# Optimization experiments

Measured on AMD Instinct MI355X. Metric: run time of the kernel, lower is better.

Reference implementation:

```python
import jax, jax.numpy as jnp
import numpy as np
import math

DIM = 1024
HEADS = 16
WINDOW = 256  # window_size; also used as block size (band covers 3 blocks)


def _rope(x):
    # canonical half-split RoPE over the FULL feature dim (as the module applies
    # it before the head split), base 10000
    b, s, d = x.shape
    half = d // 2
    inv_freq = 1.0 / (10000.0 ** (jnp.arange(half, dtype=jnp.float32) / half))
    ang = jnp.arange(s, dtype=jnp.float32)[:, None] * inv_freq[None, :]  # [s, half]
    cos, sin = jnp.cos(ang), jnp.sin(ang)
    x1, x2 = x[..., :half], x[..., half:]
    return jnp.concatenate([x1 * cos - x2 * sin, x1 * sin + x2 * cos], axis=-1)


def setup_inputs() -> dict:
    key = jax.random.key(0)
    ks = jax.random.split(key, 8)
    d = DIM
    q = jax.random.normal(ks[0], (2, 4096, d), dtype=jnp.float32)
    k = jax.random.normal(ks[1], (2, 4096, d), dtype=jnp.float32)
    v = jax.random.normal(ks[2], (2, 4096, d), dtype=jnp.float32)
    wq = jax.random.normal(ks[3], (d, d), dtype=jnp.float32) * 0.02
    wk = jax.random.normal(ks[4], (d, d), dtype=jnp.float32) * 0.02
    wv = jax.random.normal(ks[5], (d, d), dtype=jnp.float32) * 0.02
    wo_w = jax.random.normal(ks[6], (d, d), dtype=jnp.float32) * 0.02
    wo_b = jnp.zeros((d,), dtype=jnp.float32)
    return {"q": q, "k": k, "v": v, "wq": wq, "wk": wk, "wv": wv,
            "wo_w": wo_w, "wo_b": wo_b}


def reference(q, k, v, wq, wk, wv, wo_w, wo_b):
    b, s, d = q.shape
    h, W = HEADS, WINDOW
    dk = d // h
    B = W                      # block size == window -> band of 3 blocks
    nb = s // B

    # projections (torch Linear: x @ W^T), then RoPE over the full dim
    qp = _rope(jnp.einsum('bsd,ed->bse', q, wq))
    kp = _rope(jnp.einsum('bsd,ed->bse', k, wk))
    vp = jnp.einsum('bsd,ed->bse', v, wv)

    # split heads -> [b, h, s, dk]
    qh = qp.reshape(b, s, h, dk).transpose(0, 2, 1, 3)
    kh = kp.reshape(b, s, h, dk).transpose(0, 2, 1, 3)
    vh = vp.reshape(b, s, h, dk).transpose(0, 2, 1, 3)

    # pad keys/values by one block on each side, gather 3-block bands
    kpad = jnp.pad(kh, ((0, 0), (0, 0), (B, B), (0, 0)))
    vpad = jnp.pad(vh, ((0, 0), (0, 0), (B, B), (0, 0)))
    kblk = kpad.reshape(b, h, nb + 2, B, dk)
    vblk = vpad.reshape(b, h, nb + 2, B, dk)
    kband = jnp.concatenate([kblk[:, :, i:i + nb] for i in range(3)], axis=3)  # [b,h,nb,3B,dk]
    vband = jnp.concatenate([vblk[:, :, i:i + nb] for i in range(3)], axis=3)

    qb = qh.reshape(b, h, nb, B, dk)
    # NOTE: original multiplies by sqrt(dim_k) (not divides) -- kept faithfully
    scores = jnp.einsum('bhnqd,bhnkd->bhnqk', qb, kband) * math.sqrt(dk)

    # band mask: key global pos = (n-1)*B + ki, query global pos = n*B + qi
    n_idx = jnp.arange(nb)[:, None, None]
    qi = jnp.arange(B)[None, :, None]
    ki = jnp.arange(3 * B)[None, None, :]
    kpos = (n_idx - 1) * B + ki
    rel = ki - B - qi  # key_pos - query_pos
    valid = (rel >= -W) & (rel <= W) & (kpos >= 0) & (kpos < s)  # [nb,B,3B]

    neg = jnp.asarray(jnp.finfo(scores.dtype).min, scores.dtype)
    scores = jnp.where(valid[None, None], scores, neg)
    attn = jax.nn.softmax(scores, axis=-1)

    out = jnp.einsum('bhnqk,bhnkd->bhnqd', attn, vband)
    out = out.reshape(b, h, s, dk).transpose(0, 2, 1, 3).reshape(b, s, d)
    return jnp.einsum('bsd,ed->bse', out, wo_w) + wo_b
```

## Files before the change

### kernel.cpp

```cpp
#include <hip/hip_runtime.h>


typedef __attribute__((ext_vector_type(8))) short short8v;
typedef __attribute__((ext_vector_type(4))) float float4v;
typedef __attribute__((ext_vector_type(8))) _Float16 half8v;

#define MFMA_BF16(A_, B_, C_) __builtin_amdgcn_mfma_f32_16x16x32_bf16((A_), (B_), (C_), 0, 0, 0)
#define MFMA_F16(A_, B_, C_)  __builtin_amdgcn_mfma_f32_16x16x32_f16((A_), (B_), (C_), 0, 0, 0)

__device__ __forceinline__ void split_rn(float x, short& h, short& l) {
    unsigned int u = __float_as_uint(x);
    u += 0x7fffu + ((u >> 16) & 1u);
    unsigned int hb = u & 0xffff0000u;
    h = (short)(hb >> 16);
    float lo = x - __uint_as_float(hb);
    l = (short)(__float_as_uint(lo) >> 16);
}

__device__ __forceinline__ void dma16(const void* g, void* l) {
    __builtin_amdgcn_global_load_lds(
        (__attribute__((address_space(1))) void*)g,
        (__attribute__((address_space(3))) void*)l, 16, 0, 0);
}

__global__ __launch_bounds__(256) void prep_k(
    const float* __restrict__ wq, const float* __restrict__ wk,
    const float* __restrict__ wv, unsigned short* __restrict__ scr)
{
    const int M1 = 1 << 20;
    unsigned int tid = blockIdx.x * 256 + threadIdx.x;
    if (tid < (unsigned)M1) {
        short h, l; split_rn(wq[tid], h, l);
        scr[tid] = (unsigned short)h;
        scr[M1 + tid] = (unsigned short)l;
    } else if (tid < (unsigned)(2 * M1)) {
        unsigned int i = tid - M1;
        short h, l; split_rn(wk[i], h, l);
        scr[2 * M1 + i] = (unsigned short)h;
        scr[3 * M1 + i] = (unsigned short)l;
    } else {
        unsigned int i = tid - 2 * M1;
        scr[4 * M1 + i] = __builtin_bit_cast(unsigned short, (_Float16)wv[i]);
    }
}

__global__ __launch_bounds__(256) void gemm_qk(
    const float* __restrict__ A0, const short* __restrict__ Bh0,
    const short* __restrict__ Bl0, float* __restrict__ C0,
    const float* __restrict__ A1, const short* __restrict__ Bh1,
    const short* __restrict__ Bl1, float* __restrict__ C1)
{
    const int N = 1024, K = 1024;
    const float* Ap = blockIdx.z ? A1 : A0;
    const short* Bhp = blockIdx.z ? Bh1 : Bh0;
    const short* Blp = blockIdx.z ? Bl1 : Bl0;
    float*       Cp = blockIdx.z ? C1 : C0;

    __shared__ __align__(16) short Ahs[128 * 32];
    __shared__ __align__(16) short Als[128 * 32];
    __shared__ __align__(16) short Bhs[128 * 32];
    __shared__ __align__(16) short Bls[128 * 32];

    const int t = threadIdx.x;
    const int bm = blockIdx.y << 7;
    const int bn = blockIdx.x << 7;
    const int lane = t & 63;
    const int wave = t >> 6;
    const int wm = (wave >> 1) << 6;
    const int wn = (wave & 1) << 6;
    const int c16 = lane & 15;
    const int quad = lane >> 4;
    const int lr = t >> 2;
    const int lc = (t & 3) << 3;

    float4v acc[4][4];
#pragma unroll
    for (int i = 0; i < 4; i++)
#pragma unroll
        for (int j = 0; j < 4; j++) acc[i][j] = (float4v){0.f, 0.f, 0.f, 0.f};

    for (int kb = 0; kb < K; kb += 32) {
#pragma unroll
        for (int g = 0; g < 2; g++) {
            size_t off = (size_t)(bn + g * 64 + lr) * K + kb + lc;
            dma16(Bhp + off, Bhs + g * 2048 + wave * 512);
            dma16(Blp + off, Bls + g * 2048 + wave * 512);
        }
#pragma unroll
        for (int g = 0; g < 2; g++) {
            const float* src = Ap + (size_t)(bm + g * 64 + lr) * K + kb + lc;
            float4v f0 = *(const float4v*)src;
            float4v f1 = *(const float4v*)(src + 4);
            short8v h, l;
#pragma unroll
            for (int j = 0; j < 8; j++) {
                float x = (j < 4) ? f0[j] : f1[j - 4];
                short hh, ll; split_rn(x, hh, ll);
                h[j] = hh; l[j] = ll;
            }
            *(short8v*)(Ahs + (g * 64 + lr) * 32 + lc) = h;
            *(short8v*)(Als + (g * 64 + lr) * 32 + lc) = l;
        }
        __syncthreads();

        short8v ah[4], al[4], bh[4], bl[4];
#pragma unroll
        for (int i = 0; i < 4; i++) {
            ah[i] = *(const short8v*)(Ahs + (wm + i * 16 + c16) * 32 + quad * 8);
            al[i] = *(const short8v*)(Als + (wm + i * 16 + c16) * 32 + quad * 8);
        }
#pragma unroll
        for (int j = 0; j < 4; j++) {
            bh[j] = *(const short8v*)(Bhs + (wn + j * 16 + c16) * 32 + quad * 8);
            bl[j] = *(const short8v*)(Bls + (wn + j * 16 + c16) * 32 + quad * 8);
        }
#pragma unroll
        for (int i = 0; i < 4; i++)
#pragma unroll
            for (int j = 0; j < 4; j++) {
                acc[i][j] = MFMA_BF16(ah[i], bh[j], acc[i][j]);
                acc[i][j] = MFMA_BF16(ah[i], bl[j], acc[i][j]);
                acc[i][j] = MFMA_BF16(al[i], bh[j], acc[i][j]);
            }
        __syncthreads();
    }

#pragma unroll
    for (int i = 0; i < 4; i++)
#pragma unroll
        for (int j = 0; j < 4; j++)
#pragma unroll
            for (int r = 0; r < 4; r++) {
                int gr = bm + wm + i * 16 + quad * 4 + r;
                int gc = bn + wn + j * 16 + c16;
                Cp[(size_t)gr * N + gc] = acc[i][j][r];
            }
}

template <int AF16, int BF16, int OMODE>
__global__ __launch_bounds__(256) void gemm16(
    const void* __restrict__ Ap, const void* __restrict__ Bp,
    void* __restrict__ Cp, const float* __restrict__ bias)
{
    const int N = 1024, K = 1024;

    __shared__ __align__(16) short As[128 * 32];
    __shared__ __align__(16) short Bs[128 * 32];

    const int t = threadIdx.x;
    const int bm = blockIdx.y << 7;
    const int bn = blockIdx.x << 7;
    const int lane = t & 63;
    const int wave = t >> 6;
    const int wm = (wave >> 1) << 6;
    const int wn = (wave & 1) << 6;
    const int c16 = lane & 15;
    const int quad = lane >> 4;
    const int lr = t >> 2;
    const int lc = (t & 3) << 3;

    float4v acc[4][4];
#pragma unroll
    for (int i = 0; i < 4; i++)
#pragma unroll
        for (int j = 0; j < 4; j++) acc[i][j] = (float4v){0.f, 0.f, 0.f, 0.f};

    for (int kb = 0; kb < K; kb += 32) {
        if (AF16) {
            const _Float16* Af = (const _Float16*)Ap;
#pragma unroll
            for (int g = 0; g < 2; g++)
                dma16(Af + (size_t)(bm + g * 64 + lr) * K + kb + lc,
                      As + g * 2048 + wave * 512);
        } else {
            const float* Af = (const float*)Ap;
#pragma unroll
            for (int g = 0; g < 2; g++) {
                const float* src = Af + (size_t)(bm + g * 64 + lr) * K + kb + lc;
                float4v f0 = *(const float4v*)src;
                float4v f1 = *(const float4v*)(src + 4);
                half8v h;
#pragma unroll
                for (int j = 0; j < 8; j++) h[j] = (_Float16)((j < 4) ? f0[j] : f1[j - 4]);
                *(half8v*)(As + (g * 64 + lr) * 32 + lc) = h;
            }
        }
        if (BF16) {
            const _Float16* Bf = (const _Float16*)Bp;
#pragma unroll
            for (int g = 0; g < 2; g++)
                dma16(Bf + (size_t)(bn + g * 64 + lr) * K + kb + lc,
                      Bs + g * 2048 + wave * 512);
        } else {
            const float* Bf = (const float*)Bp;
#pragma unroll
            for (int g = 0; g < 2; g++) {
                const float* src = Bf + (size_t)(bn + g * 64 + lr) * K + kb + lc;
                float4v f0 = *(const float4v*)src;
                float4v f1 = *(const float4v*)(src + 4);
                half8v h;
#pragma unroll
                for (int j = 0; j < 8; j++) h[j] = (_Float16)((j < 4) ? f0[j] : f1[j - 4]);
                *(half8v*)(Bs + (g * 64 + lr) * 32 + lc) = h;
            }
        }
        __syncthreads();

        half8v ah[4], bh[4];
#pragma unroll
        for (int i = 0; i < 4; i++)
            ah[i] = *(const half8v*)(As + (wm + i * 16 + c16) * 32 + quad * 8);
#pragma unroll
        for (int j = 0; j < 4; j++)
            bh[j] = *(const half8v*)(Bs + (wn + j * 16 + c16) * 32 + quad * 8);
#pragma unroll
        for (int i = 0; i < 4; i++)
#pragma unroll
            for (int j = 0; j < 4; j++)
                acc[i][j] = MFMA_F16(ah[i], bh[j], acc[i][j]);
        __syncthreads();
    }

#pragma unroll
    for (int i = 0; i < 4; i++)
#pragma unroll
        for (int j = 0; j < 4; j++)
#pragma unroll
            for (int r = 0; r < 4; r++) {
                int gr = bm + wm + i * 16 + quad * 4 + r;
                int gc = bn + wn + j * 16 + c16;
                float vv = acc[i][j][r];
                if (OMODE == 0) {
                    ((unsigned short*)Cp)[((size_t)(gc << 1) + (gr >> 12)) * 4096 + (gr & 4095)] =
                        __builtin_bit_cast(unsigned short, (_Float16)vv);
                } else {
                    ((float*)Cp)[(size_t)gr * N + gc] = vv + bias[gc];
                }
            }
}

__global__ __launch_bounds__(256) void rope_pack(float* __restrict__ QP, float* __restrict__ KP)
{
    int sp = blockIdx.x;
    int t = threadIdx.x;
    float* rows[4] = { QP + ((size_t)sp << 10), QP + ((size_t)(4096 + sp) << 10),
                       KP + ((size_t)sp << 10), KP + ((size_t)(4096 + sp) << 10) };

    float c[2], sn[2];
    float x1[4][2], x2[4][2];
#pragma unroll
    for (int p = 0; p < 2; p++) {
        int j = t + p * 256;
        float freq = __expf(-0.017988946f * (float)j);
        float ang = (float)sp * freq;
        sincosf(ang, &sn[p], &c[p]);
#pragma unroll
        for (int r = 0; r < 4; r++) {
            x1[r][p] = rows[r][j];
            x2[r][p] = rows[r][j + 512];
        }
    }
    __syncthreads();
#pragma unroll
    for (int r = 0; r < 4; r++) {
        unsigned short* u = (unsigned short*)rows[r];
#pragma unroll
        for (int p = 0; p < 2; p++) {
            int j = t + p * 256;
            float y1 = x1[r][p] * c[p] - x2[r][p] * sn[p];
            float y2 = x1[r][p] * sn[p] + x2[r][p] * c[p];
            short h1, l1, h2, l2;
            split_rn(y1, h1, l1);
            split_rn(y2, h2, l2);
            u[j] = (unsigned short)h1;
            u[j + 512] = (unsigned short)h2;
            u[1024 + j] = (unsigned short)l1;
            u[1024 + j + 512] = (unsigned short)l2;
        }
    }
}

__global__ __launch_bounds__(256) void attn_k(
    const unsigned short* __restrict__ QHL, const unsigned short* __restrict__ KHL,
    const unsigned short* __restrict__ VT, unsigned short* __restrict__ AO)
{
    const int S = 4096;
    const float NEG = -1e30f;
    const float PSC = 512.0f;
    const int bq = blockIdx.x, h = blockIdx.y, b = blockIdx.z;
    const int t = threadIdx.x;
    const int wave = t >> 6, lane = t & 63;
    const int col = lane & 15, quad = lane >> 4;
    const int qg = (bq << 6) + (wave << 4);

    __shared__ __align__(16) short Khs[64 * 72];
    __shared__ __align__(16) short Kls[64 * 72];
    __shared__ __align__(16) short Vs[64 * 72];
    __shared__ __align__(16) short Ps[4][16 * 72];
    short* myP = &Ps[wave][0];

    const int sk = t >> 3;
    const int sd = (t & 7) << 3;

    short8v qh[2], ql[2];
    {
        const unsigned short* qr = QHL + ((size_t)(b * S + qg + col) << 11) + h * 64 + quad * 8;
        qh[0] = *(const short8v*)(qr);
        qh[1] = *(const short8v*)(qr + 32);
        ql[0] = *(const short8v*)(qr + 1024);
        ql[1] = *(const short8v*)(qr + 1024 + 32);
    }

    float mrun[4], lrun[4];
    float4v O[4];
#pragma unroll
    for (int r = 0; r < 4; r++) { mrun[r] = NEG; lrun[r] = 0.f; }
#pragma unroll
    for (int t4 = 0; t4 < 4; t4++) O[t4] = (float4v){0.f, 0.f, 0.f, 0.f};

    const int blk0 = bq << 6;
    const int kstart = (blk0 - 256 > 0) ? (blk0 - 256) : 0;
    const int kend = (blk0 + 320 < S) ? (blk0 + 320) : S;

    for (int kb = kstart; kb < kend; kb += 64) {
#pragma unroll
        for (int p = 0; p < 2; p++) {
            int key = p * 32 + sk;
            const unsigned short* krow = KHL + ((size_t)(b * S + kb + key) << 11) + h * 64 + sd;
            *(short8v*)(Khs + key * 72 + sd) = *(const short8v*)krow;
            *(short8v*)(Kls + key * 72 + sd) = *(const short8v*)(krow + 1024);
            int dm = p * 32 + sk;
            const unsigned short* vrow = VT + ((size_t)((h * 64 + dm) << 1) + b) * S + kb + sd;
            *(short8v*)(Vs + dm * 72 + sd) = *(const short8v*)vrow;
        }
        __syncthreads();

        float4v sv[4];
#pragma unroll
        for (int c = 0; c < 4; c++) {
            const short* kro = Khs + (c * 16 + col) * 72 + quad * 8;
            const short* klo = Kls + (c * 16 + col) * 72 + quad * 8;
            short8v kh0 = *(const short8v*)kro;
            short8v kh1 = *(const short8v*)(kro + 32);
            short8v kl0 = *(const short8v*)klo;
            short8v kl1 = *(const short8v*)(klo + 32);
            float4v sc = (float4v){0.f, 0.f, 0.f, 0.f};
            sc = MFMA_BF16(qh[0], kh0, sc);
            sc = MFMA_BF16(qh[1], kh1, sc);
            sc = MFMA_BF16(qh[0], kl0, sc);
            sc = MFMA_BF16(qh[1], kl1, sc);
            sc = MFMA_BF16(ql[0], kh0, sc);
            sc = MFMA_BF16(ql[1], kh1, sc);
            sv[c] = sc;
        }

        float mx[4], alpha[4], psum[4];
#pragma unroll
        for (int r = 0; r < 4; r++) {
            int qrow = qg + quad * 4 + r;
            float m = NEG;
#pragma unroll
            for (int c = 0; c < 4; c++) {
                int key = kb + c * 16 + col;
                float vv = (key >= qrow - 256 && key <= qrow + 256) ? sv[c][r] * 8.0f : NEG;
                sv[c][r] = vv;
                m = fmaxf(m, vv);
            }
            mx[r] = m;
        }
#pragma unroll
        for (int st = 1; st < 16; st <<= 1)
#pragma unroll
            for (int r = 0; r < 4; r++) mx[r] = fmaxf(mx[r], __shfl_xor(mx[r], st, 64));

#pragma unroll
        for (int r = 0; r < 4; r++) {
            float mn = fmaxf(mrun[r], mx[r]);
            alpha[r] = __expf(mrun[r] - mn);
            mrun[r] = mn;
            float ps = 0.f;
#pragma unroll
            for (int c = 0; c < 4; c++) {
                float p = __expf(sv[c][r] - mn);
                ps += p;
                myP[(quad * 4 + r) * 72 + c * 16 + col] =
                    __builtin_bit_cast(short, (_Float16)(p * PSC));
            }
            psum[r] = ps;
        }
#pragma unroll
        for (int st = 1; st < 16; st <<= 1)
#pragma unroll
            for (int r = 0; r < 4; r++) psum[r] += __shfl_xor(psum[r], st, 64);
#pragma unroll
        for (int r = 0; r < 4; r++) lrun[r] = lrun[r] * alpha[r] + psum[r];
#pragma unroll
        for (int t4 = 0; t4 < 4; t4++)
#pragma unroll
            for (int r = 0; r < 4; r++) O[t4][r] *= alpha[r];

#pragma unroll
        for (int kf = 0; kf < 2; kf++) {
            half8v pa = *(const half8v*)(myP + col * 72 + kf * 32 + quad * 8);
#pragma unroll
            for (int t4 = 0; t4 < 4; t4++) {
                half8v vb = *(const half8v*)(Vs + (t4 * 16 + col) * 72 + kf * 32 + quad * 8);
                O[t4] = MFMA_F16(pa, vb, O[t4]);
            }
        }
        __syncthreads();
    }

#pragma unroll
    for (int r = 0; r < 4; r++) {
        float inv = (lrun[r] > 0.f) ? (1.0f / (lrun[r] * PSC)) : 0.f;
        unsigned short* orow = AO + (size_t)(b * S + qg + quad * 4 + r) * 1024 + h * 64;
#pragma unroll
        for (int t4 = 0; t4 < 4; t4++)
            orow[t4 * 16 + col] = __builtin_bit_cast(unsigned short, (_Float16)(O[t4][r] * inv));
    }
}

extern "C" void kernel_launch(void* const* d_in, const int* in_sizes, int n_in,
                              void* d_out, int out_size, void* d_ws, size_t ws_size,
                              hipStream_t stream) {
    const float* q   = (const float*)d_in[0];
    const float* k   = (const float*)d_in[1];
    const float* v   = (const float*)d_in[2];
    const float* wq  = (const float*)d_in[3];
    const float* wk  = (const float*)d_in[4];
    const float* wv  = (const float*)d_in[5];
    const float* wo  = (const float*)d_in[6];
    const float* wob = (const float*)d_in[7];

    float* QP = (float*)d_ws;
    float* KP = QP + (size_t)8192 * 1024;
    unsigned short* VT = (unsigned short*)(KP + (size_t)8192 * 1024);
    unsigned short* AO = VT + (size_t)8192 * 1024;

    unsigned short* scr = (unsigned short*)d_out;
    const int M1 = 1 << 20;
    const short* wqh = (const short*)(scr);
    const short* wql = (const short*)(scr + M1);
    const short* wkh = (const short*)(scr + 2 * M1);
    const short* wkl = (const short*)(scr + 3 * M1);
    const void*  wv16 = (const void*)(scr + 4 * M1);

    prep_k<<<12288, 256, 0, stream>>>(wq, wk, wv, scr);
    gemm_qk<<<dim3(8, 64, 2), 256, 0, stream>>>(q, wqh, wql, QP, k, wkh, wkl, KP);
    rope_pack<<<4096, 256, 0, stream>>>(QP, KP);
    gemm16<0, 1, 0><<<dim3(8, 64), 256, 0, stream>>>(v, wv16, (void*)VT, nullptr);
    attn_k<<<dim3(64, 16, 2), 256, 0, stream>>>((const unsigned short*)QP,
                                                (const unsigned short*)KP, VT, AO);
    gemm16<1, 0, 1><<<dim3(8, 64), 256, 0, stream>>>(AO, wo, d_out, wob);
}
```

Measured before the change: 457.1 us.

## Rewrite split-bf16 Q/K projection GEMM with 256x256 tiles and double-buffered LDS

Replaces the 128x128 Q/K projection GEMM with a 512-thread, 256x256-tile kernel. It double-buffers LDS, prefetches the next A tile into registers and DMAs the next B tile while computing, and paces the loads with explicit vmcnt waits and barriers. It also adds an XOR swizzle to avoid LDS bank conflicts, an XCD-aware block remap, and raised MFMA priority. The goal is to hide global-load latency and raise MFMA utilisation, at the cost of higher register and LDS pressure and fragile hand-tuned wait counts.

```diff
diff --git a/kernel.cpp b/kernel.cpp
--- a/kernel.cpp
+++ b/kernel.cpp
@@ -7,6 +7,11 @@
 
 #define MFMA_BF16(A_, B_, C_) __builtin_amdgcn_mfma_f32_16x16x32_bf16((A_), (B_), (C_), 0, 0, 0)
 #define MFMA_F16(A_, B_, C_)  __builtin_amdgcn_mfma_f32_16x16x32_f16((A_), (B_), (C_), 0, 0, 0)
+
+#define VMW_(n) asm volatile("s_waitcnt vmcnt(" #n ")" ::: "memory")
+#define VMW(n) VMW_(n)
+#define LGKM0 asm volatile("s_waitcnt lgkmcnt(0)" ::: "memory")
+#define BARF do { __builtin_amdgcn_s_barrier(); asm volatile("" ::: "memory"); } while (0)
 
 __device__ __forceinline__ void split_rn(float x, short& h, short& l) {
     unsigned int u = __float_as_uint(x);
@@ -44,97 +49,187 @@
     }
 }
 
-__global__ __launch_bounds__(256) void gemm_qk(
+__global__ __launch_bounds__(512, 2) void gemm_qk2(
     const float* __restrict__ A0, const short* __restrict__ Bh0,
     const short* __restrict__ Bl0, float* __restrict__ C0,
     const float* __restrict__ A1, const short* __restrict__ Bh1,
     const short* __restrict__ Bl1, float* __restrict__ C1)
 {
-    const int N = 1024, K = 1024;
-    const float* Ap = blockIdx.z ? A1 : A0;
-    const short* Bhp = blockIdx.z ? Bh1 : Bh0;
-    const short* Blp = blockIdx.z ? Bl1 : Bl0;
-    float*       Cp = blockIdx.z ? C1 : C0;
-
-    __shared__ __align__(16) short Ahs[128 * 32];
-    __shared__ __align__(16) short Als[128 * 32];
-    __shared__ __align__(16) short Bhs[128 * 32];
-    __shared__ __align__(16) short Bls[128 * 32];
+    __shared__ __align__(16) short S[2 * 32768];
+
+    const int bid = blockIdx.x;
+    const int cid = ((bid & 7) << 5) | (bid >> 3);
+    const int z   = cid >> 7;
+    const int rem = cid & 127;
+    const int bm  = (rem >> 2) << 8;
+    const int bn  = (rem & 3) << 8;
+
+    const float* Ap  = z ? A1  : A0;
+    const short* Bhp = z ? Bh1 : Bh0;
+    const short* Blp = z ? Bl1 : Bl0;
+    float*       Cp  = z ? C1  : C0;
 
     const int t = threadIdx.x;
-    const int bm = blockIdx.y << 7;
-    const int bn = blockIdx.x << 7;
-    const int lane = t & 63;
-    const int wave = t >> 6;
-    const int wm = (wave >> 1) << 6;
-    const int wn = (wave & 1) << 6;
-    const int c16 = lane & 15;
-    const int quad = lane >> 4;
-    const int lr = t >> 2;
-    const int lc = (t & 3) << 3;
-
-    float4v acc[4][4];
-#pragma unroll
-    for (int i = 0; i < 4; i++)
+    const int wave = t >> 6, lane = t & 63;
+    const int c16 = lane & 15, quad = lane >> 4;
+    const int wm = (wave >> 2) << 7;
+    const int wn = (wave & 3) << 6;
+
+    const int ar = t >> 1;
+    const int ah16 = (t & 1) << 4;
+    const int fA = (ar & 3) ^ ((ar >> 2) & 3);
+    const int swA0 = ((((t & 1) << 1) | 0) ^ fA) << 3;
+    const int swA1 = ((((t & 1) << 1) | 1) ^ fA) << 3;
+
+    const int br  = lane >> 2;
+    const int fsl = (((lane & 3) ^ ((br & 3) ^ ((br >> 2) & 3))) << 3);
+
+    const int frd = ((quad ^ ((c16 & 3) ^ ((c16 >> 2) & 3))) << 3);
+
+    float4v acc[8][4];
+#pragma unroll
+    for (int i = 0; i < 8; i++)
 #pragma unroll
         for (int j = 0; j < 4; j++) acc[i][j] = (float4v){0.f, 0.f, 0.f, 0.f};
 
-    for (int kb = 0; kb < K; kb += 32) {
-#pragma unroll
-        for (int g = 0; g < 2; g++) {
-            size_t off = (size_t)(bn + g * 64 + lr) * K + kb + lc;
-            dma16(Bhp + off, Bhs + g * 2048 + wave * 512);
-            dma16(Blp + off, Bls + g * 2048 + wave * 512);
-        }
-#pragma unroll
-        for (int g = 0; g < 2; g++) {
-            const float* src = Ap + (size_t)(bm + g * 64 + lr) * K + kb + lc;
-            float4v f0 = *(const float4v*)src;
-            float4v f1 = *(const float4v*)(src + 4);
-            short8v h, l;
-#pragma unroll
-            for (int j = 0; j < 8; j++) {
-                float x = (j < 4) ? f0[j] : f1[j - 4];
-                short hh, ll; split_rn(x, hh, ll);
-                h[j] = hh; l[j] = ll;
-            }
-            *(short8v*)(Ahs + (g * 64 + lr) * 32 + lc) = h;
-            *(short8v*)(Als + (g * 64 + lr) * 32 + lc) = l;
-        }
-        __syncthreads();
-
-        short8v ah[4], al[4], bh[4], bl[4];
-#pragma unroll
-        for (int i = 0; i < 4; i++) {
-            ah[i] = *(const short8v*)(Ahs + (wm + i * 16 + c16) * 32 + quad * 8);
-            al[i] = *(const short8v*)(Als + (wm + i * 16 + c16) * 32 + quad * 8);
-        }
+#define STAGE_B(pp, kk)                                                          \
+    do {                                                                         \
+        const size_t rb = (size_t)(bn + (wave << 5) + br) * 1024 + (kk) + fsl;   \
+        short* dh = S + (pp) * 32768 + 16384 + (wave << 10);                     \
+        short* dl = dh + 8192;                                                   \
+        dma16(Bhp + rb,             dh);                                         \
+        dma16(Bhp + rb + 16 * 1024, dh + 512);                                   \
+        dma16(Blp + rb,             dl);                                         \
+        dma16(Blp + rb + 16 * 1024, dl + 512);                                   \
+    } while (0)
+
+    const float* arow = Ap + (size_t)(bm + ar) * 1024 + ah16;
+    float4v ap0 = *(const float4v*)(arow + 0);
+    float4v ap1 = *(const float4v*)(arow + 4);
+    float4v ap2 = *(const float4v*)(arow + 8);
+    float4v ap3 = *(const float4v*)(arow + 12);
+    STAGE_B(0, 0);
+
+#define SPLIT_WRITE(sp_)                                                         \
+    do {                                                                         \
+        short8v h0, l0, h1, l1;                                                  \
+        _Pragma("unroll")                                                        \
+        for (int jj = 0; jj < 4; jj++) {                                         \
+            short hh, ll;                                                        \
+            split_rn(ap0[jj], hh, ll); h0[jj] = hh;     l0[jj] = ll;             \
+            split_rn(ap1[jj], hh, ll); h0[jj + 4] = hh; l0[jj + 4] = ll;         \
+            split_rn(ap2[jj], hh, ll); h1[jj] = hh;     l1[jj] = ll;             \
+            split_rn(ap3[jj], hh, ll); h1[jj + 4] = hh; l1[jj + 4] = ll;         \
+        }                                                                        \
+        short* abase = (sp_) + ar * 32;                                          \
+        *(short8v*)(abase + swA0) = h0;                                          \
+        *(short8v*)(abase + swA1) = h1;                                          \
+        *(short8v*)(abase + 8192 + swA0) = l0;                                   \
+        *(short8v*)(abase + 8192 + swA1) = l1;                                   \
+    } while (0)
+
+#define LOAD_AH_BH(sp_)                                                          \
+    _Pragma("unroll")                                                            \
+    for (int i = 0; i < 8; i++)                                                  \
+        ah[i] = *(const short8v*)((sp_) + (wm + i * 16 + c16) * 32 + frd);       \
+    _Pragma("unroll")                                                            \
+    for (int j = 0; j < 4; j++)                                                  \
+        bh[j] = *(const short8v*)((sp_) + 16384 + (wn + j * 16 + c16) * 32 + frd)
+
+#define MFMA_CLUSTER(AARR, BARR)                                                 \
+    do {                                                                         \
+        __builtin_amdgcn_s_setprio(1);                                           \
+        _Pragma("unroll")                                                        \
+        for (int i = 0; i < 8; i++)                                              \
+            _Pragma("unroll")                                                    \
+            for (int j = 0; j < 4; j++)                                          \
+                acc[i][j] = MFMA_BF16(AARR[i & 7], BARR[j & 3], acc[i][j]);      \
+        __builtin_amdgcn_s_setprio(0);                                           \
+    } while (0)
+
+    int kb = 0;
+#pragma unroll 1
+    for (int tt = 0; tt < 31; ++tt, kb += 32) {
+        const int p = tt & 1;
+        short* sp = S + p * 32768;
+
+        VMW(4);
+        SPLIT_WRITE(sp);
+        ap0 = *(const float4v*)(arow + kb + 32);
+        ap1 = *(const float4v*)(arow + kb + 36);
+        ap2 = *(const float4v*)(arow + kb + 40);
+        ap3 = *(const float4v*)(arow + kb + 44);
+        LGKM0;
+        BARF;
+        STAGE_B(p ^ 1, kb + 32);
+        VMW(10);
+        BARF;
+        short8v ah[8], bh[4];
+        LOAD_AH_BH(sp);
+        MFMA_CLUSTER(ah, bh);
+        VMW(8);
+        BARF;
+        {
+            short8v bl[4];
+#pragma unroll
+            for (int j = 0; j < 4; j++)
+                bl[j] = *(const short8v*)(sp + 24576 + (wn + j * 16 + c16) * 32 + frd);
+            MFMA_CLUSTER(ah, bl);
+        }
+        {
+            short8v al[8];
+#pragma unroll
+            for (int i = 0; i < 8; i++)
+                al[i] = *(const short8v*)(sp + 8192 + (wm + i * 16 + c16) * 32 + frd);
+            MFMA_CLUSTER(al, bh);
+        }
+    }
+
+    {
+        short* sp = S + 32768;
+        VMW(4);
+        SPLIT_WRITE(sp);
+        LGKM0;
+        BARF;
+        VMW(2);
+        BARF;
+        short8v ah[8], bh[4];
+        LOAD_AH_BH(sp);
+        MFMA_CLUSTER(ah, bh);
+        VMW(0);
+        BARF;
+        {
+            short8v bl[4];
+#pragma unroll
+            for (int j = 0; j < 4; j++)
+                bl[j] = *(const short8v*)(sp + 24576 + (wn + j * 16 + c16) * 32 + frd);
+            MFMA_CLUSTER(ah, bl);
+        }
+        {
+            short8v al[8];
+#pragma unroll
+            for (int i = 0; i < 8; i++)
+                al[i] = *(const short8v*)(sp + 8192 + (wm + i * 16 + c16) * 32 + frd);
+            MFMA_CLUSTER(al, bh);
+        }
+    }
+
+#undef STAGE_B
+#undef SPLIT_WRITE
+#undef LOAD_AH_BH
+#undef MFMA_CLUSTER
+
+#pragma unroll
+    for (int i = 0; i < 8; i++) {
+        const size_t gr0 = (size_t)(bm + wm + i * 16 + quad * 4);
 #pragma unroll
         for (int j = 0; j < 4; j++) {
-            bh[j] = *(const short8v*)(Bhs + (wn + j * 16 + c16) * 32 + quad * 8);
-            bl[j] = *(const short8v*)(Bls + (wn + j * 16 + c16) * 32 + quad * 8);
-        }
-#pragma unroll
-        for (int i = 0; i < 4; i++)
-#pragma unroll
-            for (int j = 0; j < 4; j++) {
-                acc[i][j] = MFMA_BF16(ah[i], bh[j], acc[i][j]);
-                acc[i][j] = MFMA_BF16(ah[i], bl[j], acc[i][j]);
-                acc[i][j] = MFMA_BF16(al[i], bh[j], acc[i][j]);
-            }
-        __syncthreads();
-    }
-
-#pragma unroll
-    for (int i = 0; i < 4; i++)
-#pragma unroll
-        for (int j = 0; j < 4; j++)
-#pragma unroll
-            for (int r = 0; r < 4; r++) {
-                int gr = bm + wm + i * 16 + quad * 4 + r;
-                int gc = bn + wn + j * 16 + c16;
-                Cp[(size_t)gr * N + gc] = acc[i][j][r];
-            }
+            const int gc = bn + wn + j * 16 + c16;
+#pragma unroll
+            for (int r = 0; r < 4; r++)
+                Cp[(gr0 + r) * 1024 + gc] = acc[i][j][r];
+        }
+    }
 }
 
 template <int AF16, int BF16, int OMODE>
@@ -447,7 +542,7 @@
     const void*  wv16 = (const void*)(scr + 4 * M1);
 
     prep_k<<<12288, 256, 0, stream>>>(wq, wk, wv, scr);
-    gemm_qk<<<dim3(8, 64, 2), 256, 0, stream>>>(q, wqh, wql, QP, k, wkh, wkl, KP);
+    gemm_qk2<<<256, 512, 0, stream>>>(q, wqh, wql, QP, k, wkh, wkl, KP);
     rope_pack<<<4096, 256, 0, stream>>>(QP, KP);
     gemm16<0, 1, 0><<<dim3(8, 64), 256, 0, stream>>>(v, wv16, (void*)VT, nullptr);
     attn_k<<<dim3(64, 16, 2), 256, 0, stream>>>((const unsigned short*)QP,
```

After: 429.7 us. -6.0%, faster.
